# Optimization experiments

Hardware: AMD Instinct MI355X
Metric: run time of the kernel (lower is better)

## Reference

```python
import jax, jax.numpy as jnp
import numpy as np

KH, KW = 7, 7            # extraction kernel
EH, EW = 5, 5            # effective (cropped) kernel
PAD = (KH - EH) // 2     # = 1
EPS = 1e-7


def _extract_patches(x):
    # x: [B,H,W,C] -> patches [B,Ho,Wo,KH,KW,C], stride 1, VALID padding
    B, H, Wd, C = x.shape
    Ho, Wo = H - KH + 1, Wd - KW + 1
    rows = []
    for i in range(KH):
        cols = [x[:, i:i + Ho, j:j + Wo, :] for j in range(KW)]
        rows.append(jnp.stack(cols, axis=3))          # [B,Ho,Wo,KW,C]
    return jnp.stack(rows, axis=3)                     # [B,Ho,Wo,KH,KW,C]


def _rotate_bilinear(patches, angles):
    # patches: [N,KH,KW,C]; angles: [N]. Mirrors tf.contrib.image
    # angles_to_projective_transforms + transform(BILINEAR, fill=0).
    # Note: the layer's det(matrix)==0 NEAREST fallback never fires (det==1).
    N = patches.shape[0]
    c, s = jnp.cos(angles), jnp.sin(angles)
    Wm1, Hm1 = jnp.float32(KW - 1), jnp.float32(KH - 1)
    xo = (Wm1 - (c * Wm1 - s * Hm1)) * 0.5
    yo = (Hm1 - (s * Wm1 + c * Hm1)) * 0.5
    scale = jnp.float32(1.0 + EPS)   # transforms /= transforms[:,8:9]+1e-7
    a0, a1, a2 = c / scale, -s / scale, xo / scale
    a3, a4, a5 = s / scale, c / scale, yo / scale
    yg, xg = jnp.meshgrid(jnp.arange(KH, dtype=jnp.float32),
                          jnp.arange(KW, dtype=jnp.float32), indexing='ij')
    x_in = a0[:, None, None] * xg + a1[:, None, None] * yg + a2[:, None, None]
    y_in = a3[:, None, None] * xg + a4[:, None, None] * yg + a5[:, None, None]
    x0f = jnp.floor(x_in); y0f = jnp.floor(y_in)
    wx1 = x_in - x0f; wx0 = 1.0 - wx1
    wy1 = y_in - y0f; wy0 = 1.0 - wy1
    x0 = x0f.astype(jnp.int32); x1 = x0 + 1
    y0 = y0f.astype(jnp.int32); y1 = y0 + 1
    nidx = jnp.arange(N)[:, None, None]

    def corner(yi, xi, w):
        valid = ((xi >= 0) & (xi < KW) & (yi >= 0) & (yi < KH)).astype(patches.dtype)
        v = patches[nidx, jnp.clip(yi, 0, KH - 1), jnp.clip(xi, 0, KW - 1)]
        return (w * valid)[..., None] * v

    return (corner(y0, x0, wy0 * wx0) + corner(y0, x1, wy0 * wx1) +
            corner(y1, x0, wy1 * wx0) + corner(y1, x1, wy1 * wx1))


def reference(x, W, b):
    B, H, Wd, C = x.shape
    patches = _extract_patches(x)                      # [B,Ho,Wo,KH,KW,C]
    _, Ho, Wo = patches.shape[:3]
    intensity = jnp.sum(patches, axis=-1)              # [B,Ho,Wo,KH,KW]
    row_idx = jnp.repeat(jnp.arange(KH, dtype=jnp.float32), KW)   # rowMulti
    col_idx = jnp.tile(jnp.arange(KW, dtype=jnp.float32), KH)     # colMulti
    flat = intensity.reshape(-1, KH * KW)              # [N, KH*KW]
    denom = jnp.sum(flat, -1) + EPS
    cr = jnp.sum(flat * row_idx, -1) / denom - (KH - 1) / 2.0
    cc = jnp.sum(flat * col_idx, -1) / denom - (KW - 1) / 2.0
    angle = jnp.arctan2(cr, cc + EPS)                  # [N]
    patches_n = patches.reshape(-1, KH, KW, C)         # [N,KH,KW,C]
    rot = _rotate_bilinear(patches_n, angle)
    rot = rot[:, PAD:PAD + EH, PAD:PAD + EW, :]        # crop to effective
    rot = rot.reshape(B, Ho, Wo, EH * EW * C)
    w_flat = W.reshape(W.shape[0], -1)                 # [F, EH*EW*C]
    out = jnp.einsum('bhwk,fk->bhwf', rot, w_flat) + b
    return out


def setup_inputs() -> dict:
    key = jax.random.key(0)
    kx, kw, _ = jax.random.split(key, 3)
    x = jax.random.normal(kx, (8, 64, 64, 32), dtype=jnp.float32)
    W = jax.random.normal(kw, (64, EH, EW, 32), dtype=jnp.float32) * 0.05
    b = jnp.zeros((64,), dtype=jnp.float32)
    return {"x": x, "W": W, "b": b}
```

## Files before the change

### kernel.cpp

```cpp
#include <hip/hip_runtime.h>
#include <hip/hip_bf16.h>

#define EPSF 1e-7f
#define B_ 8
#define H_ 64
#define W_ 64
#define C_ 32
#define HO 58
#define WO 58
#define NF 64
#define KDIM 800

#define XBS 40
#define RS  808

typedef __bf16 v8bf __attribute__((ext_vector_type(8)));
typedef float  v4f  __attribute__((ext_vector_type(4)));
typedef float  v2f  __attribute__((ext_vector_type(2)));

__global__ void k_wpack(const float* __restrict__ W, __bf16* __restrict__ Wp) {
    int t = blockIdx.x*256 + threadIdx.x;
    int j = t & 7; int lane = (t >> 3) & 63; int rest = t >> 9;
    int kb = rest % 25; int nt = rest / 25;
    int f = nt*16 + (lane & 15);
    int k = kb*32 + (lane >> 4)*8 + j;
    Wp[t] = (__bf16)W[f*KDIM + k];
}

__global__ __launch_bounds__(256, 4)
void k_main(const float* __restrict__ x, const v8bf* __restrict__ Wp,
            const float* __restrict__ bias, float* __restrict__ out) {
    __shared__ __bf16 xtb[7][22][XBS];
    __shared__ __bf16 rot[16][RS];
    __shared__ float  Srow[7][22];

    int tid = threadIdx.x;
    int wv = tid >> 6, lane = tid & 63;
    int m = lane & 15, q = lane >> 4;

    int L = blockIdx.x + 4*(blockIdx.y + 58*blockIdx.z);
    int newL = (L & 7)*232 + (L >> 3);
    int b  = newL / 232;
    int rem = newL - b*232;
    int ho = rem >> 2;
    int wt = rem & 3;

    int wo0 = wt*16;
    int npx = WO - wo0; if (npx > 16) npx = 16;
    int ncols = npx + 6;

    float bv = bias[wv*16 + m];

    if (tid < 7*ncols) {
        int r, c;
        if (ncols == 22) { r = tid/22; c = tid - r*22; }
        else             { r = tid >> 4; c = tid & 15; }
        const float* src = x + (size_t)((b*H_ + ho + r)*W_ + wo0 + c)*C_;
        float4 vq[8];
#pragma unroll
        for (int qq = 0; qq < 8; qq++) vq[qq] = *(const float4*)(src + qq*4);
        float s = 0.f;
#pragma unroll
        for (int qq = 0; qq < 8; qq++) s += vq[qq].x + vq[qq].y + vq[qq].z + vq[qq].w;
        Srow[r][c] = s;
#pragma unroll
        for (int h8 = 0; h8 < 4; h8++) {
            v8bf o;
            o[0]=(__bf16)vq[h8*2].x;   o[1]=(__bf16)vq[h8*2].y;
            o[2]=(__bf16)vq[h8*2].z;   o[3]=(__bf16)vq[h8*2].w;
            o[4]=(__bf16)vq[h8*2+1].x; o[5]=(__bf16)vq[h8*2+1].y;
            o[6]=(__bf16)vq[h8*2+1].z; o[7]=(__bf16)vq[h8*2+1].w;
            *(v8bf*)&xtb[r][c][h8*8] = o;
        }
    }
    __syncthreads();

    int pxl = wv*4 + q;
    float den = 0.f, crn = 0.f, ccn = 0.f;
#pragma unroll
    for (int k = 0; k < 4; k++) {
        int t = m + 16*k;
        if (t < 49) {
            int i = t / 7, j = t - 7*i;
            float v = Srow[i][pxl + j];
            den += v; crn += v*(float)i; ccn += v*(float)j;
        }
    }
#pragma unroll
    for (int msk = 1; msk <= 8; msk <<= 1) {
        den += __shfl_xor(den, msk);
        crn += __shfl_xor(crn, msk);
        ccn += __shfl_xor(ccn, msk);
    }
    float pc, ps, pxo, pyo;
    {
        float dt = den + EPSF;
        float cr = crn/dt - 3.0f;
        float cx = ccn/dt - 3.0f + EPSF;
        float r2 = cr*cr + cx*cx;
        float inv = r2 > 0.f ? rsqrtf(r2) : 0.f;
        float c = r2 > 0.f ? cx*inv : 1.0f;
        float s = cr*inv;
        const float scale = 1.0f + EPSF;
        pc  = c/scale; ps = s/scale;
        pxo = (6.0f - (c*6.0f - s*6.0f))*0.5f/scale;
        pyo = (6.0f - (s*6.0f + c*6.0f))*0.5f/scale;
    }

#pragma unroll
    for (int rnd = 0; rnd < 2; rnd++) {
        int pos = m + 16*rnd;
        if (pos < 25) {
            int py = pos/5; int yy = py + 1; int xx = pos - py*5 + 1;
            float xin = pc*(float)xx - ps*(float)yy + pxo;
            float yin = ps*(float)xx + pc*(float)yy + pyo;
            float x0f = floorf(xin), y0f = floorf(yin);
            float wx1 = xin - x0f, wx0 = 1.0f - wx1;
            float wy1 = yin - y0f, wy0 = 1.0f - wy1;
            int ix0 = (int)x0f, iy0 = (int)y0f;
            int ix1 = ix0 + 1,  iy1 = iy0 + 1;

            const __bf16* bp[4]; float wgt[4];
            auto mkcorner = [&](int yi, int xi, float w, int idx) {
                bool valid = (xi >= 0) & (xi < 7) & (yi >= 0) & (yi < 7);
                int cy = yi < 0 ? 0 : (yi > 6 ? 6 : yi);
                int cx2 = xi < 0 ? 0 : (xi > 6 ? 6 : xi);
                bp[idx]  = &xtb[cy][pxl + cx2][0];
                wgt[idx] = valid ? w : 0.0f;
            };
            mkcorner(iy0, ix0, wy0*wx0, 0);
            mkcorner(iy0, ix1, wy0*wx1, 1);
            mkcorner(iy1, ix0, wy1*wx0, 2);
            mkcorner(iy1, ix1, wy1*wx1, 3);

            v2f acc[16];
#pragma unroll
            for (int i = 0; i < 16; i++) acc[i] = (v2f){0.f, 0.f};
#pragma unroll
            for (int cn = 0; cn < 4; cn++) {
                const __bf16* src = bp[cn];
                v2f wq2 = (v2f){wgt[cn], wgt[cn]};
#pragma unroll
                for (int q8 = 0; q8 < 4; q8++) {
                    union { v8bf v; unsigned u[4]; } uv;
                    uv.v = *(const v8bf*)(src + q8*8);
#pragma unroll
                    for (int d = 0; d < 4; d++) {
                        v2f val = (v2f){ __uint_as_float(uv.u[d] << 16),
                                         __uint_as_float(uv.u[d] & 0xffff0000u) };
                        acc[q8*4 + d] += wq2 * val;
                    }
                }
            }
#pragma unroll
            for (int q8 = 0; q8 < 4; q8++) {
                v8bf o;
#pragma unroll
                for (int d = 0; d < 4; d++) {
                    o[2*d]   = (__bf16)acc[q8*4 + d].x;
                    o[2*d+1] = (__bf16)acc[q8*4 + d].y;
                }
                *(v8bf*)&rot[pxl][pos*32 + q8*8] = o;
            }
        }
    }

    const v8bf* wp = Wp + (size_t)wv*25*64 + lane;
    v8bf bfA[13];
#pragma unroll
    for (int kb = 0; kb < 13; kb++) bfA[kb] = wp[kb*64];
    __syncthreads();

    v8bf bfB[12];
#pragma unroll
    for (int kb = 0; kb < 12; kb++) bfB[kb] = wp[(13 + kb)*64];

    v4f acc0 = {0.f, 0.f, 0.f, 0.f};
    v4f acc1 = {0.f, 0.f, 0.f, 0.f};
#pragma unroll
    for (int kb = 0; kb < 12; kb++) {
        v8bf a0 = *(const v8bf*)&rot[m][kb*32 + q*8];
        acc0 = __builtin_amdgcn_mfma_f32_16x16x32_bf16(a0, bfA[kb], acc0, 0, 0, 0);
        v8bf a1 = *(const v8bf*)&rot[m][(13 + kb)*32 + q*8];
        acc1 = __builtin_amdgcn_mfma_f32_16x16x32_bf16(a1, bfB[kb], acc1, 0, 0, 0);
    }
    {
        v8bf a0 = *(const v8bf*)&rot[m][12*32 + q*8];
        acc0 = __builtin_amdgcn_mfma_f32_16x16x32_bf16(a0, bfA[12], acc0, 0, 0, 0);
    }

    int f = wv*16 + m;
    int pixbase = (b*HO + ho)*WO + wo0;
#pragma unroll
    for (int r = 0; r < 4; r++) {
        int px = q*4 + r;
        if (px < npx) out[(size_t)(pixbase + px)*NF + f] = acc0[r] + acc1[r] + bv;
    }
}

extern "C" void kernel_launch(void* const* d_in, const int* in_sizes, int n_in,
                              void* d_out, int out_size, void* d_ws, size_t ws_size,
                              hipStream_t stream) {
    const float* x    = (const float*)d_in[0];
    const float* W    = (const float*)d_in[1];
    const float* bias = (const float*)d_in[2];
    float* out = (float*)d_out;
    __bf16* Wp = (__bf16*)d_ws;

    k_wpack<<<dim3(200), 256, 0, stream>>>(W, Wp);
    k_main<<<dim3(4, HO, B_), 256, 0, stream>>>(x, (const v8bf*)Wp, bias, out);
}
```

Baseline: 76.17 us.

## Halve rotated-patch LDS buffer by two-phase rotate/MFMA and split input loads

Splits the 25 rotated positions into two phases (13 then 12) that reuse a half-sized rot buffer, running MFMAs after each phase with two extra barriers. The smaller LDS footprint lets launch bounds target five blocks per CU instead of four. The input tile load is also split into half-channel work items so more threads take part, with partial row sums summed afterwards. The cost is added synchronization and a tighter register budget from the higher occupancy target, which could cause spills.

```diff
diff --git a/kernel.cpp b/kernel.cpp
--- a/kernel.cpp
+++ b/kernel.cpp
@@ -12,7 +12,7 @@
 #define KDIM 800
 
 #define XBS 40
-#define RS  808
+#define RS  424
 
 typedef __bf16 v8bf __attribute__((ext_vector_type(8)));
 typedef float  v4f  __attribute__((ext_vector_type(4)));
@@ -27,12 +27,12 @@
     Wp[t] = (__bf16)W[f*KDIM + k];
 }
 
-__global__ __launch_bounds__(256, 4)
+__global__ __launch_bounds__(256, 5)
 void k_main(const float* __restrict__ x, const v8bf* __restrict__ Wp,
             const float* __restrict__ bias, float* __restrict__ out) {
     __shared__ __bf16 xtb[7][22][XBS];
     __shared__ __bf16 rot[16][RS];
-    __shared__ float  Srow[7][22];
+    __shared__ float  SrowH[2][7][22];
 
     int tid = threadIdx.x;
     int wv = tid >> 6, lane = tid & 63;
@@ -51,26 +51,31 @@
 
     float bv = bias[wv*16 + m];
 
-    if (tid < 7*ncols) {
-        int r, c;
-        if (ncols == 22) { r = tid/22; c = tid - r*22; }
-        else             { r = tid >> 4; c = tid & 15; }
-        const float* src = x + (size_t)((b*H_ + ho + r)*W_ + wo0 + c)*C_;
-        float4 vq[8];
-#pragma unroll
-        for (int qq = 0; qq < 8; qq++) vq[qq] = *(const float4*)(src + qq*4);
-        float s = 0.f;
-#pragma unroll
-        for (int qq = 0; qq < 8; qq++) s += vq[qq].x + vq[qq].y + vq[qq].z + vq[qq].w;
-        Srow[r][c] = s;
-#pragma unroll
-        for (int h8 = 0; h8 < 4; h8++) {
-            v8bf o;
-            o[0]=(__bf16)vq[h8*2].x;   o[1]=(__bf16)vq[h8*2].y;
-            o[2]=(__bf16)vq[h8*2].z;   o[3]=(__bf16)vq[h8*2].w;
-            o[4]=(__bf16)vq[h8*2+1].x; o[5]=(__bf16)vq[h8*2+1].y;
-            o[6]=(__bf16)vq[h8*2+1].z; o[7]=(__bf16)vq[h8*2+1].w;
-            *(v8bf*)&xtb[r][c][h8*8] = o;
+    {
+        int items = 7*ncols*2;
+        const float* xb = x + (size_t)((b*H_ + ho)*W_ + wo0)*C_;
+        for (int e = tid; e < items; e += 256) {
+            int h = e & 1; int rc = e >> 1;
+            int r, c;
+            if (ncols == 22) { r = rc/22; c = rc - r*22; }
+            else             { r = rc >> 4; c = rc & 15; }
+            const float* src = xb + (size_t)(r*W_ + c)*C_ + h*16;
+            float4 vq[4];
+#pragma unroll
+            for (int qq = 0; qq < 4; qq++) vq[qq] = *(const float4*)(src + qq*4);
+            float s = 0.f;
+#pragma unroll
+            for (int qq = 0; qq < 4; qq++) s += vq[qq].x + vq[qq].y + vq[qq].z + vq[qq].w;
+            SrowH[h][r][c] = s;
+#pragma unroll
+            for (int h8 = 0; h8 < 2; h8++) {
+                v8bf o;
+                o[0]=(__bf16)vq[h8*2].x;   o[1]=(__bf16)vq[h8*2].y;
+                o[2]=(__bf16)vq[h8*2].z;   o[3]=(__bf16)vq[h8*2].w;
+                o[4]=(__bf16)vq[h8*2+1].x; o[5]=(__bf16)vq[h8*2+1].y;
+                o[6]=(__bf16)vq[h8*2+1].z; o[7]=(__bf16)vq[h8*2+1].w;
+                *(v8bf*)&xtb[r][c][h*16 + h8*8] = o;
+            }
         }
     }
     __syncthreads();
@@ -82,7 +87,7 @@
         int t = m + 16*k;
         if (t < 49) {
             int i = t / 7, j = t - 7*i;
-            float v = Srow[i][pxl + j];
+            float v = SrowH[0][i][pxl + j] + SrowH[1][i][pxl + j];
             den += v; crn += v*(float)i; ccn += v*(float)j;
         }
     }
@@ -107,86 +112,87 @@
         pyo = (6.0f - (s*6.0f + c*6.0f))*0.5f/scale;
     }
 
-#pragma unroll
-    for (int rnd = 0; rnd < 2; rnd++) {
-        int pos = m + 16*rnd;
-        if (pos < 25) {
-            int py = pos/5; int yy = py + 1; int xx = pos - py*5 + 1;
-            float xin = pc*(float)xx - ps*(float)yy + pxo;
-            float yin = ps*(float)xx + pc*(float)yy + pyo;
-            float x0f = floorf(xin), y0f = floorf(yin);
-            float wx1 = xin - x0f, wx0 = 1.0f - wx1;
-            float wy1 = yin - y0f, wy0 = 1.0f - wy1;
-            int ix0 = (int)x0f, iy0 = (int)y0f;
-            int ix1 = ix0 + 1,  iy1 = iy0 + 1;
-
-            const __bf16* bp[4]; float wgt[4];
-            auto mkcorner = [&](int yi, int xi, float w, int idx) {
-                bool valid = (xi >= 0) & (xi < 7) & (yi >= 0) & (yi < 7);
-                int cy = yi < 0 ? 0 : (yi > 6 ? 6 : yi);
-                int cx2 = xi < 0 ? 0 : (xi > 6 ? 6 : xi);
-                bp[idx]  = &xtb[cy][pxl + cx2][0];
-                wgt[idx] = valid ? w : 0.0f;
-            };
-            mkcorner(iy0, ix0, wy0*wx0, 0);
-            mkcorner(iy0, ix1, wy0*wx1, 1);
-            mkcorner(iy1, ix0, wy1*wx0, 2);
-            mkcorner(iy1, ix1, wy1*wx1, 3);
-
-            v2f acc[16];
-#pragma unroll
-            for (int i = 0; i < 16; i++) acc[i] = (v2f){0.f, 0.f};
-#pragma unroll
-            for (int cn = 0; cn < 4; cn++) {
-                const __bf16* src = bp[cn];
-                v2f wq2 = (v2f){wgt[cn], wgt[cn]};
-#pragma unroll
-                for (int q8 = 0; q8 < 4; q8++) {
-                    union { v8bf v; unsigned u[4]; } uv;
-                    uv.v = *(const v8bf*)(src + q8*8);
-#pragma unroll
-                    for (int d = 0; d < 4; d++) {
-                        v2f val = (v2f){ __uint_as_float(uv.u[d] << 16),
-                                         __uint_as_float(uv.u[d] & 0xffff0000u) };
-                        acc[q8*4 + d] += wq2 * val;
-                    }
+    auto do_rot = [&](int pos, int slot) {
+        int py = pos/5; int yy = py + 1; int xx = pos - py*5 + 1;
+        float xin = pc*(float)xx - ps*(float)yy + pxo;
+        float yin = ps*(float)xx + pc*(float)yy + pyo;
+        float x0f = floorf(xin), y0f = floorf(yin);
+        float wx1 = xin - x0f, wx0 = 1.0f - wx1;
+        float wy1 = yin - y0f, wy0 = 1.0f - wy1;
+        int ix0 = (int)x0f, iy0 = (int)y0f;
+        int ix1 = ix0 + 1,  iy1 = iy0 + 1;
+
+        const __bf16* bp[4]; float wgt[4];
+        auto mkcorner = [&](int yi, int xi, float w, int idx) {
+            bool valid = (xi >= 0) & (xi < 7) & (yi >= 0) & (yi < 7);
+            int cy = yi < 0 ? 0 : (yi > 6 ? 6 : yi);
+            int cx2 = xi < 0 ? 0 : (xi > 6 ? 6 : xi);
+            bp[idx]  = &xtb[cy][pxl + cx2][0];
+            wgt[idx] = valid ? w : 0.0f;
+        };
+        mkcorner(iy0, ix0, wy0*wx0, 0);
+        mkcorner(iy0, ix1, wy0*wx1, 1);
+        mkcorner(iy1, ix0, wy1*wx0, 2);
+        mkcorner(iy1, ix1, wy1*wx1, 3);
+
+        v2f acc[16];
+#pragma unroll
+        for (int i = 0; i < 16; i++) acc[i] = (v2f){0.f, 0.f};
+#pragma unroll
+        for (int cn = 0; cn < 4; cn++) {
+            const __bf16* src = bp[cn];
+            v2f wq2 = (v2f){wgt[cn], wgt[cn]};
+#pragma unroll
+            for (int q8 = 0; q8 < 4; q8++) {
+                union { v8bf v; unsigned u[4]; } uv;
+                uv.v = *(const v8bf*)(src + q8*8);
+#pragma unroll
+                for (int d = 0; d < 4; d++) {
+                    v2f val = (v2f){ __uint_as_float(uv.u[d] << 16),
+                                     __uint_as_float(uv.u[d] & 0xffff0000u) };
+                    acc[q8*4 + d] += wq2 * val;
                 }
             }
-#pragma unroll
-            for (int q8 = 0; q8 < 4; q8++) {
-                v8bf o;
-#pragma unroll
-                for (int d = 0; d < 4; d++) {
-                    o[2*d]   = (__bf16)acc[q8*4 + d].x;
-                    o[2*d+1] = (__bf16)acc[q8*4 + d].y;
-                }
-                *(v8bf*)&rot[pxl][pos*32 + q8*8] = o;
+        }
+#pragma unroll
+        for (int q8 = 0; q8 < 4; q8++) {
+            v8bf o;
+#pragma unroll
+            for (int d = 0; d < 4; d++) {
+                o[2*d]   = (__bf16)acc[q8*4 + d].x;
+                o[2*d+1] = (__bf16)acc[q8*4 + d].y;
             }
-        }
-    }
+            *(v8bf*)&rot[pxl][slot*32 + q8*8] = o;
+        }
+    };
 
     const v8bf* wp = Wp + (size_t)wv*25*64 + lane;
-    v8bf bfA[13];
-#pragma unroll
-    for (int kb = 0; kb < 13; kb++) bfA[kb] = wp[kb*64];
-    __syncthreads();
-
-    v8bf bfB[12];
-#pragma unroll
-    for (int kb = 0; kb < 12; kb++) bfB[kb] = wp[(13 + kb)*64];
-
     v4f acc0 = {0.f, 0.f, 0.f, 0.f};
     v4f acc1 = {0.f, 0.f, 0.f, 0.f};
+
+    if (m < 13) do_rot(m, m);
+    v8bf bfA[13];
+#pragma unroll
+    for (int kb = 0; kb < 13; kb++) bfA[kb] = wp[kb*64];
+    __syncthreads();
+#pragma unroll
+    for (int kb = 0; kb < 13; kb++) {
+        v8bf a = *(const v8bf*)&rot[m][kb*32 + q*8];
+        if (kb & 1) acc1 = __builtin_amdgcn_mfma_f32_16x16x32_bf16(a, bfA[kb], acc1, 0, 0, 0);
+        else        acc0 = __builtin_amdgcn_mfma_f32_16x16x32_bf16(a, bfA[kb], acc0, 0, 0, 0);
+    }
+    __syncthreads();
+
+    if (m < 12) do_rot(13 + m, m);
+    v8bf bfB[12];
+#pragma unroll
+    for (int kb = 0; kb < 12; kb++) bfB[kb] = wp[(13 + kb)*64];
+    __syncthreads();
 #pragma unroll
     for (int kb = 0; kb < 12; kb++) {
-        v8bf a0 = *(const v8bf*)&rot[m][kb*32 + q*8];
-        acc0 = __builtin_amdgcn_mfma_f32_16x16x32_bf16(a0, bfA[kb], acc0, 0, 0, 0);
-        v8bf a1 = *(const v8bf*)&rot[m][(13 + kb)*32 + q*8];
-        acc1 = __builtin_amdgcn_mfma_f32_16x16x32_bf16(a1, bfB[kb], acc1, 0, 0, 0);
-    }
-    {
-        v8bf a0 = *(const v8bf*)&rot[m][12*32 + q*8];
-        acc0 = __builtin_amdgcn_mfma_f32_16x16x32_bf16(a0, bfA[12], acc0, 0, 0, 0);
+        v8bf a = *(const v8bf*)&rot[m][kb*32 + q*8];
+        if (kb & 1) acc1 = __builtin_amdgcn_mfma_f32_16x16x32_bf16(a, bfB[kb], acc1, 0, 0, 0);
+        else        acc0 = __builtin_amdgcn_mfma_f32_16x16x32_bf16(a, bfB[kb], acc0, 0, 0, 0);
     }
 
     int f = wv*16 + m;
```

New measurement: 76.50 us. About the same (+0.4%).

## Process two output rows per block to reuse input halo and weight fragments

Applied to the files above, without the earlier changes.

Each block now handles two consecutive output rows, loading an 8-row input strip once and keeping all 25 weight fragments in registers for both rows. The angle computation is reorganized so each lane group computes one row's centroid, and parameters are exchanged via shuffles. This halves the grid and reduces redundant halo and weight loads, at the cost of higher register pressure (launch bounds lowered to 3), extra syncthreads, and serialized rotate/MFMA phases per row.

```diff
diff --git a/kernel.cpp b/kernel.cpp
--- a/kernel.cpp
+++ b/kernel.cpp
@@ -27,23 +27,24 @@
     Wp[t] = (__bf16)W[f*KDIM + k];
 }
 
-__global__ __launch_bounds__(256, 4)
+__global__ __launch_bounds__(256, 3)
 void k_main(const float* __restrict__ x, const v8bf* __restrict__ Wp,
             const float* __restrict__ bias, float* __restrict__ out) {
-    __shared__ __bf16 xtb[7][22][XBS];
+    __shared__ __bf16 xtb[8][22][XBS];
     __shared__ __bf16 rot[16][RS];
-    __shared__ float  Srow[7][22];
+    __shared__ float  Srow[8][22];
 
     int tid = threadIdx.x;
     int wv = tid >> 6, lane = tid & 63;
     int m = lane & 15, q = lane >> 4;
 
-    int L = blockIdx.x + 4*(blockIdx.y + 58*blockIdx.z);
-    int newL = (L & 7)*232 + (L >> 3);
-    int b  = newL / 232;
-    int rem = newL - b*232;
-    int ho = rem >> 2;
-    int wt = rem & 3;
+    int L = blockIdx.x + 4*(blockIdx.y + 29*blockIdx.z);
+    int newL = (L & 7)*116 + (L >> 3);
+    int b   = newL / 116;
+    int rem = newL - b*116;
+    int hog = rem >> 2;
+    int wt  = rem & 3;
+    int ho0 = hog*2;
 
     int wo0 = wt*16;
     int npx = WO - wo0; if (npx > 16) npx = 16;
@@ -51,11 +52,11 @@
 
     float bv = bias[wv*16 + m];
 
-    if (tid < 7*ncols) {
+    if (tid < 8*ncols) {
         int r, c;
         if (ncols == 22) { r = tid/22; c = tid - r*22; }
         else             { r = tid >> 4; c = tid & 15; }
-        const float* src = x + (size_t)((b*H_ + ho + r)*W_ + wo0 + c)*C_;
+        const float* src = x + (size_t)((b*H_ + ho0 + r)*W_ + wo0 + c)*C_;
         float4 vq[8];
 #pragma unroll
         for (int qq = 0; qq < 8; qq++) vq[qq] = *(const float4*)(src + qq*4);
@@ -75,19 +76,20 @@
     }
     __syncthreads();
 
-    int pxl = wv*4 + q;
+    int slot = lane & 7;
+    int g = (lane >> 3) & 7;
+    int myT = g & 1;
+    int myC = wv*4 + (g >> 1);
     float den = 0.f, crn = 0.f, ccn = 0.f;
-#pragma unroll
-    for (int k = 0; k < 4; k++) {
-        int t = m + 16*k;
-        if (t < 49) {
-            int i = t / 7, j = t - 7*i;
-            float v = Srow[i][pxl + j];
-            den += v; crn += v*(float)i; ccn += v*(float)j;
-        }
-    }
-#pragma unroll
-    for (int msk = 1; msk <= 8; msk <<= 1) {
+    if (slot < 7) {
+#pragma unroll
+        for (int j = 0; j < 7; j++) {
+            float v = Srow[myT + slot][myC + j];
+            den += v; crn += v*(float)slot; ccn += v*(float)j;
+        }
+    }
+#pragma unroll
+    for (int msk = 1; msk <= 4; msk <<= 1) {
         den += __shfl_xor(den, msk);
         crn += __shfl_xor(crn, msk);
         ccn += __shfl_xor(ccn, msk);
@@ -106,95 +108,112 @@
         pxo = (6.0f - (c*6.0f - s*6.0f))*0.5f/scale;
         pyo = (6.0f - (s*6.0f + c*6.0f))*0.5f/scale;
     }
+    float pc2  = __shfl_xor(pc, 8),  ps2  = __shfl_xor(ps, 8);
+    float pxo2 = __shfl_xor(pxo, 8), pyo2 = __shfl_xor(pyo, 8);
+
+    auto do_rot = [&](int t, int pos, float c_, float s_, float xo_, float yo_) {
+        int pxl = wv*4 + q;
+        int py = pos/5; int yy = py + 1; int xx = pos - py*5 + 1;
+        float xin = c_*(float)xx - s_*(float)yy + xo_;
+        float yin = s_*(float)xx + c_*(float)yy + yo_;
+        float x0f = floorf(xin), y0f = floorf(yin);
+        float wx1 = xin - x0f, wx0 = 1.0f - wx1;
+        float wy1 = yin - y0f, wy0 = 1.0f - wy1;
+        int ix0 = (int)x0f, iy0 = (int)y0f;
+        int ix1 = ix0 + 1,  iy1 = iy0 + 1;
+
+        const __bf16* bp[4]; float wgt[4];
+        auto mkcorner = [&](int yi, int xi, float w, int idx) {
+            bool valid = (xi >= 0) & (xi < 7) & (yi >= 0) & (yi < 7);
+            int cy = yi < 0 ? 0 : (yi > 6 ? 6 : yi);
+            int cx2 = xi < 0 ? 0 : (xi > 6 ? 6 : xi);
+            bp[idx]  = &xtb[t + cy][pxl + cx2][0];
+            wgt[idx] = valid ? w : 0.0f;
+        };
+        mkcorner(iy0, ix0, wy0*wx0, 0);
+        mkcorner(iy0, ix1, wy0*wx1, 1);
+        mkcorner(iy1, ix0, wy1*wx0, 2);
+        mkcorner(iy1, ix1, wy1*wx1, 3);
+
+        v2f acc[16];
+#pragma unroll
+        for (int i = 0; i < 16; i++) acc[i] = (v2f){0.f, 0.f};
+#pragma unroll
+        for (int cn = 0; cn < 4; cn++) {
+            const __bf16* src = bp[cn];
+            v2f wq2 = (v2f){wgt[cn], wgt[cn]};
+#pragma unroll
+            for (int q8 = 0; q8 < 4; q8++) {
+                union { v8bf v; unsigned u[4]; } uv;
+                uv.v = *(const v8bf*)(src + q8*8);
+#pragma unroll
+                for (int d = 0; d < 4; d++) {
+                    v2f val = (v2f){ __uint_as_float(uv.u[d] << 16),
+                                     __uint_as_float(uv.u[d] & 0xffff0000u) };
+                    acc[q8*4 + d] += wq2 * val;
+                }
+            }
+        }
+#pragma unroll
+        for (int q8 = 0; q8 < 4; q8++) {
+            v8bf o;
+#pragma unroll
+            for (int d = 0; d < 4; d++) {
+                o[2*d]   = (__bf16)acc[q8*4 + d].x;
+                o[2*d+1] = (__bf16)acc[q8*4 + d].y;
+            }
+            *(v8bf*)&rot[pxl][pos*32 + q8*8] = o;
+        }
+    };
+
+    float c0 = (myT == 0) ? pc : pc2,   s0 = (myT == 0) ? ps : ps2;
+    float xo0 = (myT == 0) ? pxo : pxo2, yo0 = (myT == 0) ? pyo : pyo2;
+    float c1 = (myT == 1) ? pc : pc2,   s1 = (myT == 1) ? ps : ps2;
+    float xo1 = (myT == 1) ? pxo : pxo2, yo1 = (myT == 1) ? pyo : pyo2;
+
+    const v8bf* wp = Wp + (size_t)wv*25*64 + lane;
+    v8bf bfrag[25];
+#pragma unroll
+    for (int kb = 0; kb < 25; kb++) bfrag[kb] = wp[kb*64];
+
+    v4f accT0 = {0.f, 0.f, 0.f, 0.f};
+    v4f accT1 = {0.f, 0.f, 0.f, 0.f};
 
 #pragma unroll
     for (int rnd = 0; rnd < 2; rnd++) {
         int pos = m + 16*rnd;
-        if (pos < 25) {
-            int py = pos/5; int yy = py + 1; int xx = pos - py*5 + 1;
-            float xin = pc*(float)xx - ps*(float)yy + pxo;
-            float yin = ps*(float)xx + pc*(float)yy + pyo;
-            float x0f = floorf(xin), y0f = floorf(yin);
-            float wx1 = xin - x0f, wx0 = 1.0f - wx1;
-            float wy1 = yin - y0f, wy0 = 1.0f - wy1;
-            int ix0 = (int)x0f, iy0 = (int)y0f;
-            int ix1 = ix0 + 1,  iy1 = iy0 + 1;
-
-            const __bf16* bp[4]; float wgt[4];
-            auto mkcorner = [&](int yi, int xi, float w, int idx) {
-                bool valid = (xi >= 0) & (xi < 7) & (yi >= 0) & (yi < 7);
-                int cy = yi < 0 ? 0 : (yi > 6 ? 6 : yi);
-                int cx2 = xi < 0 ? 0 : (xi > 6 ? 6 : xi);
-                bp[idx]  = &xtb[cy][pxl + cx2][0];
-                wgt[idx] = valid ? w : 0.0f;
-            };
-            mkcorner(iy0, ix0, wy0*wx0, 0);
-            mkcorner(iy0, ix1, wy0*wx1, 1);
-            mkcorner(iy1, ix0, wy1*wx0, 2);
-            mkcorner(iy1, ix1, wy1*wx1, 3);
-
-            v2f acc[16];
-#pragma unroll
-            for (int i = 0; i < 16; i++) acc[i] = (v2f){0.f, 0.f};
-#pragma unroll
-            for (int cn = 0; cn < 4; cn++) {
-                const __bf16* src = bp[cn];
-                v2f wq2 = (v2f){wgt[cn], wgt[cn]};
-#pragma unroll
-                for (int q8 = 0; q8 < 4; q8++) {
-                    union { v8bf v; unsigned u[4]; } uv;
-                    uv.v = *(const v8bf*)(src + q8*8);
-#pragma unroll
-                    for (int d = 0; d < 4; d++) {
-                        v2f val = (v2f){ __uint_as_float(uv.u[d] << 16),
-                                         __uint_as_float(uv.u[d] & 0xffff0000u) };
-                        acc[q8*4 + d] += wq2 * val;
-                    }
-                }
-            }
-#pragma unroll
-            for (int q8 = 0; q8 < 4; q8++) {
-                v8bf o;
-#pragma unroll
-                for (int d = 0; d < 4; d++) {
-                    o[2*d]   = (__bf16)acc[q8*4 + d].x;
-                    o[2*d+1] = (__bf16)acc[q8*4 + d].y;
-                }
-                *(v8bf*)&rot[pxl][pos*32 + q8*8] = o;
-            }
-        }
-    }
-
-    const v8bf* wp = Wp + (size_t)wv*25*64 + lane;
-    v8bf bfA[13];
-#pragma unroll
-    for (int kb = 0; kb < 13; kb++) bfA[kb] = wp[kb*64];
-    __syncthreads();
-
-    v8bf bfB[12];
-#pragma unroll
-    for (int kb = 0; kb < 12; kb++) bfB[kb] = wp[(13 + kb)*64];
-
-    v4f acc0 = {0.f, 0.f, 0.f, 0.f};
-    v4f acc1 = {0.f, 0.f, 0.f, 0.f};
-#pragma unroll
-    for (int kb = 0; kb < 12; kb++) {
-        v8bf a0 = *(const v8bf*)&rot[m][kb*32 + q*8];
-        acc0 = __builtin_amdgcn_mfma_f32_16x16x32_bf16(a0, bfA[kb], acc0, 0, 0, 0);
-        v8bf a1 = *(const v8bf*)&rot[m][(13 + kb)*32 + q*8];
-        acc1 = __builtin_amdgcn_mfma_f32_16x16x32_bf16(a1, bfB[kb], acc1, 0, 0, 0);
-    }
-    {
-        v8bf a0 = *(const v8bf*)&rot[m][12*32 + q*8];
-        acc0 = __builtin_amdgcn_mfma_f32_16x16x32_bf16(a0, bfA[12], acc0, 0, 0, 0);
+        if (pos < 25) do_rot(0, pos, c0, s0, xo0, yo0);
+    }
+    __syncthreads();
+#pragma unroll
+    for (int kb = 0; kb < 25; kb++) {
+        v8bf a = *(const v8bf*)&rot[m][kb*32 + q*8];
+        accT0 = __builtin_amdgcn_mfma_f32_16x16x32_bf16(a, bfrag[kb], accT0, 0, 0, 0);
+    }
+    __syncthreads();
+
+#pragma unroll
+    for (int rnd = 0; rnd < 2; rnd++) {
+        int pos = m + 16*rnd;
+        if (pos < 25) do_rot(1, pos, c1, s1, xo1, yo1);
+    }
+    __syncthreads();
+#pragma unroll
+    for (int kb = 0; kb < 25; kb++) {
+        v8bf a = *(const v8bf*)&rot[m][kb*32 + q*8];
+        accT1 = __builtin_amdgcn_mfma_f32_16x16x32_bf16(a, bfrag[kb], accT1, 0, 0, 0);
     }
 
     int f = wv*16 + m;
-    int pixbase = (b*HO + ho)*WO + wo0;
+    int pixbase0 = (b*HO + ho0)*WO + wo0;
+    int pixbase1 = pixbase0 + WO;
 #pragma unroll
     for (int r = 0; r < 4; r++) {
         int px = q*4 + r;
-        if (px < npx) out[(size_t)(pixbase + px)*NF + f] = acc0[r] + acc1[r] + bv;
+        if (px < npx) {
+            out[(size_t)(pixbase0 + px)*NF + f] = accT0[r] + bv;
+            out[(size_t)(pixbase1 + px)*NF + f] = accT1[r] + bv;
+        }
     }
 }
 
@@ -208,5 +227,5 @@
     __bf16* Wp = (__bf16*)d_ws;
 
     k_wpack<<<dim3(200), 256, 0, stream>>>(W, Wp);
-    k_main<<<dim3(4, HO, B_), 256, 0, stream>>>(x, (const v8bf*)Wp, bias, out);
+    k_main<<<dim3(4, 29, B_), 256, 0, stream>>>(x, (const v8bf*)Wp, bias, out);
 }
```

New measurement: 109.0 us. +43.1%, slower.
